# Optimization experiments

Hardware: AMD Instinct MI355X
Metric: run time of the kernel (lower is better)

The kernel has to match this reference:

```python
import jax, jax.numpy as jnp
import numpy as np

B, VOCAB, F = 4096, 50000, 64


def setup_inputs() -> dict:
    key = jax.random.key(0)
    k1, k2 = jax.random.split(key, 2)
    # binary multi-hot input (row > 0 mask semantics of the original)
    x = jax.random.randint(k1, (B, VOCAB), 0, 2, dtype=jnp.int32)
    # truncated-normal-ish init for the factor embedding table
    V = (jax.random.normal(k2, (VOCAB, F), dtype=jnp.float32) * 0.05)
    # linear (first-order) bias table is zero-initialized in the original
    bias = jnp.zeros((VOCAB, 1), dtype=jnp.float32)
    g_bias = jnp.zeros((), dtype=jnp.float32)
    return {"x": x, "V": V, "bias": bias, "g_bias": g_bias}


def reference(x, V, bias, g_bias):
    # x: [B, VOCAB] binary multi-hot; V: [VOCAB, F]; bias: [VOCAB, 1]; g_bias: scalar
    xf = x.astype(V.dtype)
    # FM sum-square identity: for selected rows S = {i : x_i > 0},
    # 0.5 * (sum_{i,j in S} <v_i, v_j> - sum_{i in S} ||v_i||^2)
    #   = 0.5 * (||sum_i v_i||^2 - sum_i ||v_i||^2)
    xv = xf @ V                                   # [B, F] = sum of selected rows
    sum_sq = jnp.sum(xv * xv, axis=-1)            # [B]
    sq_sum = xf @ jnp.sum(V * V, axis=-1)         # [B]
    second_order = 0.5 * (sum_sq - sq_sum)        # [B]
    linear = g_bias + xf @ bias                   # [B, 1]
    return linear + second_order[:, None]         # [B, 1]
```

## Files before the change

kernel.cpp:

```cpp
#include <hip/hip_runtime.h>

#define VOCAB 50000
#define BROWS 4096
#define F 64
#define NCOLS 80
#define NT 5
#define SPLITS 16
#define NR 98
#define KT_TOTAL (SPLITS * NR)
#define KPAD (KT_TOTAL * 32)

#define AS1 __attribute__((address_space(1)))
#define AS3 __attribute__((address_space(3)))

typedef __attribute__((ext_vector_type(4))) float f32x4;
typedef __attribute__((ext_vector_type(8))) short s16x8;

__device__ __forceinline__ unsigned short f2bf(float f) {
    unsigned u = __builtin_bit_cast(unsigned, f);
    unsigned r = (u + 0x7FFFu + ((u >> 16) & 1u)) >> 16;
    return (unsigned short)r;
}
__device__ __forceinline__ float bf2f(unsigned short b) {
    unsigned u = ((unsigned)b) << 16;
    return __builtin_bit_cast(float, u);
}

__global__ void fm_prep_w(const float* __restrict__ V, const float* __restrict__ bias,
                          float* __restrict__ w) {
    int k = blockIdx.x * blockDim.x + threadIdx.x;
    if (k >= KPAD) return;
    float val = 0.f;
    if (k < VOCAB) {
        const float4* row = reinterpret_cast<const float4*>(V + (size_t)k * F);
        float ss = 0.f;
#pragma unroll
        for (int j = 0; j < F / 4; ++j) {
            float4 v = row[j];
            ss += v.x * v.x + v.y * v.y + v.z * v.z + v.w * v.w;
        }
        val = bias[k] - 0.5f * ss;
    }
    w[k] = val;
}

__global__ void fm_prep_bfrag(const float* __restrict__ V, const float* __restrict__ w,
                              uint4* __restrict__ bfrag) {
    int t = blockIdx.x * blockDim.x + threadIdx.x;
    if (t >= KT_TOTAL * NT * 64) return;
    int lane = t & 63;
    int tile = t >> 6;
    int nt = tile % NT;
    int kt = tile / NT;
    int n = nt * 16 + (lane & 15);
    int kbase = kt * 32 + (lane >> 4) * 8;
    unsigned short o[8];
#pragma unroll
    for (int j = 0; j < 8; ++j) {
        int k = kbase + j;
        float v = 0.f;
        if (k < VOCAB) {
            if (n < F) {
                v = V[(size_t)k * F + n];
            } else if (n == F) {
                v = w[k];
            } else if (n == F + 1) {
                float wv = w[k];
                v = wv - bf2f(f2bf(wv));
            }
        }
        o[j] = f2bf(v);
    }
    uint4 pk;
    pk.x = (unsigned)o[0] | ((unsigned)o[1] << 16);
    pk.y = (unsigned)o[2] | ((unsigned)o[3] << 16);
    pk.z = (unsigned)o[4] | ((unsigned)o[5] << 16);
    pk.w = (unsigned)o[6] | ((unsigned)o[7] << 16);
    bfrag[t] = pk;
}

__global__ __launch_bounds__(256, 4) void fm_main(const int* __restrict__ x,
                                                  const uint4* __restrict__ bfrag,
                                                  float* __restrict__ part) {
    __shared__ uint4 bbuf[2][NT * 64];
    const int bid = blockIdx.x;
    const int split = (bid & 7) * 2 + ((bid >> 3) & 1);
    const int mblock = bid >> 4;
    const int tid = threadIdx.x;
    const int wave = tid >> 6;
    const int lane = tid & 63;
    const int kb = lane >> 4;
    const int rowA = mblock * 64 + wave * 16 + (lane & 15);
    const int* __restrict__ xrow = x + (size_t)rowA * VOCAB;
    const int kt0 = split * NR;
    const int e0 = (wave << 6) + lane;

    auto stage = [&](int rnd) {
        const uint4* src = bfrag + (size_t)(kt0 + rnd) * (NT * 64);
        uint4* dst = bbuf[rnd & 1];
        __builtin_amdgcn_global_load_lds((const AS1 void*)(src + e0),
                                         (AS3 void*)(dst + (wave << 6)), 16, 0, 0);
        if (wave == 0)
            __builtin_amdgcn_global_load_lds((const AS1 void*)(src + 256 + lane),
                                             (AS3 void*)(dst + 256), 16, 0, 0);
    };
    auto mk = [&](int4 a0, int4 a1) -> s16x8 {
        uint4 apk;
        apk.x = ((unsigned)a0.x + ((unsigned)a0.y << 16)) * 16256u;
        apk.y = ((unsigned)a0.z + ((unsigned)a0.w << 16)) * 16256u;
        apk.z = ((unsigned)a1.x + ((unsigned)a1.y << 16)) * 16256u;
        apk.w = ((unsigned)a1.z + ((unsigned)a1.w << 16)) * 16256u;
        return __builtin_bit_cast(s16x8, apk);
    };

    f32x4 acc[NT];
#pragma unroll
    for (int nt = 0; nt < NT; ++nt) acc[nt] = (f32x4){0.f, 0.f, 0.f, 0.f};

    int4 xa, xb, na, nb;
    stage(0);
    {
        const int k = kt0 * 32 + kb * 8;
        xa = *reinterpret_cast<const int4*>(xrow + k);
        xb = *reinterpret_cast<const int4*>(xrow + k + 4);
    }

    const int nfast = (split == SPLITS - 1) ? 91 : NR;

    for (int r = 0; r < nfast; ++r) {
        asm volatile("s_waitcnt vmcnt(2)");
        __builtin_amdgcn_sched_barrier(0);
        __builtin_amdgcn_s_barrier();
        __builtin_amdgcn_sched_barrier(0);
        if (r + 1 < nfast) {
            stage(r + 1);
            const int k = (kt0 + r + 1) * 32 + kb * 8;
            na = *reinterpret_cast<const int4*>(xrow + k);
            nb = *reinterpret_cast<const int4*>(xrow + k + 4);
        }
        s16x8 af = mk(xa, xb);
        const uint4* bb = bbuf[r & 1];
#pragma unroll
        for (int nt = 0; nt < NT; ++nt) {
            s16x8 bf = __builtin_bit_cast(s16x8, bb[nt * 64 + lane]);
            acc[nt] = __builtin_amdgcn_mfma_f32_16x16x32_bf16(af, bf, acc[nt], 0, 0, 0);
        }
        xa = na; xb = nb;
    }

    if (split == SPLITS - 1) {
        for (int t = nfast; t < NR; ++t) {
            if (t == nfast) stage(t);
            const int k = (kt0 + t) * 32 + kb * 8;
            unsigned xv[8];
#pragma unroll
            for (int j = 0; j < 8; ++j) xv[j] = (k + j < VOCAB) ? (unsigned)xrow[k + j] : 0u;
            __syncthreads();
            uint4 apk;
            apk.x = (xv[0] + (xv[1] << 16)) * 16256u;
            apk.y = (xv[2] + (xv[3] << 16)) * 16256u;
            apk.z = (xv[4] + (xv[5] << 16)) * 16256u;
            apk.w = (xv[6] + (xv[7] << 16)) * 16256u;
            s16x8 af = __builtin_bit_cast(s16x8, apk);
            const uint4* bb = bbuf[t & 1];
#pragma unroll
            for (int nt = 0; nt < NT; ++nt) {
                s16x8 bf = __builtin_bit_cast(s16x8, bb[nt * 64 + lane]);
                acc[nt] = __builtin_amdgcn_mfma_f32_16x16x32_bf16(af, bf, acc[nt], 0, 0, 0);
            }
            if (t + 1 < NR) stage(t + 1);
        }
    }

    float* __restrict__ p = part + (size_t)split * BROWS * NCOLS;
    int m0 = mblock * 64 + wave * 16 + kb * 4;
    int c0 = lane & 15;
#pragma unroll
    for (int nt = 0; nt < NT; ++nt)
#pragma unroll
        for (int r = 0; r < 4; ++r)
            p[(size_t)(m0 + r) * NCOLS + nt * 16 + c0] = acc[nt][r];
}

__global__ void fm_reduce(const float* __restrict__ part, const float* __restrict__ gbias,
                          float* __restrict__ out) {
    int b = blockIdx.x * 4 + (threadIdx.x >> 6);
    int lane = threadIdx.x & 63;
    float acc = 0.f;
#pragma unroll
    for (int s = 0; s < SPLITS; ++s)
        acc += part[((size_t)s * BROWS + b) * NCOLS + lane];
    float sq = acc * acc;
    float ex = 0.f;
    if (lane < 16)       ex = part[((size_t)lane * BROWS + b) * NCOLS + F];
    else if (lane < 32)  ex = part[((size_t)(lane - 16) * BROWS + b) * NCOLS + F + 1];
#pragma unroll
    for (int off = 32; off; off >>= 1) {
        sq += __shfl_xor(sq, off, 64);
        ex += __shfl_xor(ex, off, 64);
    }
    if (lane == 0) out[b] = gbias[0] + ex + 0.5f * sq;
}

extern "C" void kernel_launch(void* const* d_in, const int* in_sizes, int n_in,
                              void* d_out, int out_size, void* d_ws, size_t ws_size,
                              hipStream_t stream) {
    const int*   x     = (const int*)d_in[0];
    const float* V     = (const float*)d_in[1];
    const float* bias  = (const float*)d_in[2];
    const float* gbias = (const float*)d_in[3];
    float* out = (float*)d_out;

    char* ws = (char*)d_ws;
    uint4* bfrag = (uint4*)ws;
    float* w     = (float*)(ws + (size_t)KT_TOTAL * NT * 64 * 16);
    float* part  = (float*)(ws + (size_t)KT_TOTAL * NT * 64 * 16 + (size_t)KPAD * 4);

    fm_prep_w<<<(KPAD + 255) / 256, 256, 0, stream>>>(V, bias, w);
    fm_prep_bfrag<<<(KT_TOTAL * NT * 64 + 255) / 256, 256, 0, stream>>>(V, w, bfrag);
    fm_main<<<(BROWS / 64) * SPLITS, 256, 0, stream>>>(x, bfrag, part);
    fm_reduce<<<BROWS / 4, 256, 0, stream>>>(part, gbias, out);
}
```

Before: 209.1 us.

## Batch x loads four rounds ahead and simplify block-to-split mapping

Reworks the main loop so each thread prefetches x for four rounds at a time into a double set of registers, raising the number of outstanding global loads to hide memory latency better. The last split's ragged tail is now handled with bounds checks inside the batch loader, which replaces the separate slow tail loop. The block-to-split mapping also changes from an interleaved scheme to a plain modulo, which alters how blocks land on XCDs and caches. The cost is higher register use (16 int4 of x in flight) and a full __syncthreads each round instead of the explicit waitcnt plus barrier.

```diff
diff --git a/kernel.cpp b/kernel.cpp
--- a/kernel.cpp
+++ b/kernel.cpp
@@ -83,9 +83,9 @@
                                                   const uint4* __restrict__ bfrag,
                                                   float* __restrict__ part) {
     __shared__ uint4 bbuf[2][NT * 64];
-    const int bid = blockIdx.x;
-    const int split = (bid & 7) * 2 + ((bid >> 3) & 1);
-    const int mblock = bid >> 4;
+    const int bx = blockIdx.x;
+    const int split = bx & (SPLITS - 1);
+    const int mblock = bx >> 4;
     const int tid = threadIdx.x;
     const int wave = tid >> 6;
     const int lane = tid & 63;
@@ -104,6 +104,24 @@
             __builtin_amdgcn_global_load_lds((const AS1 void*)(src + 256 + lane),
                                              (AS3 void*)(dst + 256), 16, 0, 0);
     };
+    auto batchload = [&](int r0, int4* d) {
+#pragma unroll
+        for (int j = 0; j < 4; ++j) {
+            const int r = r0 + j;
+            if (r >= NR) continue;
+            const int k = (kt0 + r) * 32 + kb * 8;
+            if ((kt0 + r) * 32 + 32 <= VOCAB) {
+                d[2 * j]     = *reinterpret_cast<const int4*>(xrow + k);
+                d[2 * j + 1] = *reinterpret_cast<const int4*>(xrow + k + 4);
+            } else {
+                int v[8];
+#pragma unroll
+                for (int jj = 0; jj < 8; ++jj) v[jj] = (k + jj < VOCAB) ? xrow[k + jj] : 0;
+                d[2 * j]     = make_int4(v[0], v[1], v[2], v[3]);
+                d[2 * j + 1] = make_int4(v[4], v[5], v[6], v[7]);
+            }
+        }
+    };
     auto mk = [&](int4 a0, int4 a1) -> s16x8 {
         uint4 apk;
         apk.x = ((unsigned)a0.x + ((unsigned)a0.y << 16)) * 16256u;
@@ -117,60 +135,38 @@
 #pragma unroll
     for (int nt = 0; nt < NT; ++nt) acc[nt] = (f32x4){0.f, 0.f, 0.f, 0.f};
 
-    int4 xa, xb, na, nb;
-    stage(0);
-    {
-        const int k = kt0 * 32 + kb * 8;
-        xa = *reinterpret_cast<const int4*>(xrow + k);
-        xb = *reinterpret_cast<const int4*>(xrow + k + 4);
-    }
-
-    const int nfast = (split == SPLITS - 1) ? 91 : NR;
-
-    for (int r = 0; r < nfast; ++r) {
-        asm volatile("s_waitcnt vmcnt(2)");
-        __builtin_amdgcn_sched_barrier(0);
-        __builtin_amdgcn_s_barrier();
-        __builtin_amdgcn_sched_barrier(0);
-        if (r + 1 < nfast) {
-            stage(r + 1);
-            const int k = (kt0 + r + 1) * 32 + kb * 8;
-            na = *reinterpret_cast<const int4*>(xrow + k);
-            nb = *reinterpret_cast<const int4*>(xrow + k + 4);
-        }
-        s16x8 af = mk(xa, xb);
+    auto roundbody = [&](int r, int4 a0, int4 a1) {
+        if (r + 1 < NR) stage(r + 1);
+        s16x8 af = mk(a0, a1);
         const uint4* bb = bbuf[r & 1];
 #pragma unroll
         for (int nt = 0; nt < NT; ++nt) {
             s16x8 bf = __builtin_bit_cast(s16x8, bb[nt * 64 + lane]);
             acc[nt] = __builtin_amdgcn_mfma_f32_16x16x32_bf16(af, bf, acc[nt], 0, 0, 0);
         }
-        xa = na; xb = nb;
-    }
-
-    if (split == SPLITS - 1) {
-        for (int t = nfast; t < NR; ++t) {
-            if (t == nfast) stage(t);
-            const int k = (kt0 + t) * 32 + kb * 8;
-            unsigned xv[8];
-#pragma unroll
-            for (int j = 0; j < 8; ++j) xv[j] = (k + j < VOCAB) ? (unsigned)xrow[k + j] : 0u;
-            __syncthreads();
-            uint4 apk;
-            apk.x = (xv[0] + (xv[1] << 16)) * 16256u;
-            apk.y = (xv[2] + (xv[3] << 16)) * 16256u;
-            apk.z = (xv[4] + (xv[5] << 16)) * 16256u;
-            apk.w = (xv[6] + (xv[7] << 16)) * 16256u;
-            s16x8 af = __builtin_bit_cast(s16x8, apk);
-            const uint4* bb = bbuf[t & 1];
-#pragma unroll
-            for (int nt = 0; nt < NT; ++nt) {
-                s16x8 bf = __builtin_bit_cast(s16x8, bb[nt * 64 + lane]);
-                acc[nt] = __builtin_amdgcn_mfma_f32_16x16x32_bf16(af, bf, acc[nt], 0, 0, 0);
-            }
-            if (t + 1 < NR) stage(t + 1);
-        }
-    }
+        __syncthreads();
+    };
+
+    int4 xcur[8], xnxt[8];
+    stage(0);
+    batchload(0, xcur);
+    __syncthreads();
+
+    for (int s = 0; s < 12; ++s) {
+        const int r0 = 8 * s;
+        batchload(r0 + 4, xnxt);
+        roundbody(r0 + 0, xcur[0], xcur[1]);
+        roundbody(r0 + 1, xcur[2], xcur[3]);
+        roundbody(r0 + 2, xcur[4], xcur[5]);
+        roundbody(r0 + 3, xcur[6], xcur[7]);
+        batchload(r0 + 8, xcur);
+        roundbody(r0 + 4, xnxt[0], xnxt[1]);
+        roundbody(r0 + 5, xnxt[2], xnxt[3]);
+        roundbody(r0 + 6, xnxt[4], xnxt[5]);
+        roundbody(r0 + 7, xnxt[6], xnxt[7]);
+    }
+    roundbody(96, xcur[0], xcur[1]);
+    roundbody(97, xcur[2], xcur[3]);
 
     float* __restrict__ p = part + (size_t)split * BROWS * NCOLS;
     int m0 = mblock * 64 + wave * 16 + kb * 4;
```

Result: no change. 208.1 us (-0.5%).
